# Kernel optimization log

Measured on AMD Instinct MI355X. Metric: run time of the kernel, lower is better.

Reference implementation:

```python
import jax, jax.numpy as jnp
import numpy as np

PHI = (1.0 + 5.0 ** 0.5) / 2.0
TWO_PI = 2.0 * np.pi
LN_EPS = 1e-5


def _complex_linear(xr, xi, Wr, Wi, br, bi):
    # (Wr + i*Wi) @ (xr + i*xi) + (br + i*bi)
    yr = xr @ Wr.T - xi @ Wi.T + br
    yi = xr @ Wi.T + xi @ Wr.T + bi
    return yr, yi


def _layernorm(x, g, b):
    m = jnp.mean(x, axis=-1, keepdims=True)
    v = jnp.mean((x - m) ** 2, axis=-1, keepdims=True)
    return (x - m) * jax.lax.rsqrt(v + LN_EPS) * g + b


def reference(w, b, ip_Wr, ip_Wi, ip_br, ip_bi, ln_g, ln_b, W_qkv, log_alpha, op_Wr, op_Wi):
    B, S, D = w.shape
    H = log_alpha.shape[0]
    Dh = D // H
    scale = jnp.sqrt(jnp.asarray(Dh, w.dtype))
    alpha = jax.nn.sigmoid(log_alpha)[None, :, None]  # (1,H,1)
    ts = jnp.arange(S, dtype=w.dtype)

    def step(carry, xs):
        hr, hi, vs = carry          # (B,D),(B,D),(B,H,Dh)
        w_t, b_t, t = xs            # (B,D),(B,D),()
        # InstrumentedEulerTransform: separated theta, complex product
        wl = 1.0 + jnp.abs(w_t)
        tphi = (t * PHI) % TWO_PI   # wrap_time_periodic
        thr = hr / wl + b_t + tphi
        thi = hi / wl + b_t + tphi
        sr, cr = jnp.sin(thr), jnp.cos(thr)
        si, ci = jnp.sin(thi), jnp.cos(thi)
        hr2 = cr * ci - sr * si
        hi2 = cr * si + sr * ci
        # InstrumentedEchoChamber.forward_step
        pr, pi_ = _complex_linear(hr2, hi2, ip_Wr, ip_Wi, ip_br, ip_bi)
        xc = _layernorm(pr + pi_, ln_g, ln_b)
        qkv = (xc @ W_qkv.T).reshape(B, 3, H, Dh)
        q, k, v = qkv[:, 0], qkv[:, 1], qkv[:, 2]
        vs2 = alpha * v + (1.0 - alpha) * vs
        gate = jax.nn.sigmoid(jnp.sum(q * k, axis=-1, keepdims=True) / scale)
        retr = (gate * vs2).reshape(B, D)
        # output_proj ComplexLinear on (retr, 0), no bias
        ore = retr @ op_Wr.T
        oim = retr @ op_Wi.T
        return (hr2, hi2, vs2), (ore, oim)

    init = (jnp.zeros((B, D), w.dtype), jnp.zeros((B, D), w.dtype),
            jnp.zeros((B, H, Dh), w.dtype))
    wT = jnp.swapaxes(w, 0, 1)  # (S,B,D)
    bT = jnp.swapaxes(b, 0, 1)
    _, (or_seq, oi_seq) = jax.lax.scan(step, init, (wT, bT, ts))
    out = jnp.stack([or_seq, oi_seq])      # (2,S,B,D)
    return jnp.swapaxes(out, 1, 2)         # (2,B,S,D)


def setup_inputs() -> dict:
    key = jax.random.key(0)
    ks = jax.random.split(key, 10)
    B, S, D, H = 8, 2048, 512, 8
    s = 0.02
    return {
        "w": jax.random.normal(ks[0], (B, S, D), jnp.float32),
        "b": jax.random.normal(ks[1], (B, S, D), jnp.float32),
        "ip_Wr": jax.random.normal(ks[2], (D, D), jnp.float32) * s,
        "ip_Wi": jax.random.normal(ks[3], (D, D), jnp.float32) * s,
        "ip_br": jax.random.normal(ks[4], (D,), jnp.float32) * s,
        "ip_bi": jax.random.normal(ks[5], (D,), jnp.float32) * s,
        "ln_g": jnp.ones((D,), jnp.float32),
        "ln_b": jnp.zeros((D,), jnp.float32),
        "W_qkv": jax.random.normal(ks[6], (3 * D, D), jnp.float32) * s,
        "log_alpha": jax.random.normal(ks[7], (H,), jnp.float32),
        "op_Wr": jax.random.normal(ks[8], (D, D), jnp.float32) * s,
        "op_Wi": jax.random.normal(ks[9], (D, D), jnp.float32) * s,
    }
```

## Files before the change

### kernel.cpp

```cpp
#include <hip/hip_runtime.h>
#include <math.h>

#define BB 8
#define SS 2048
#define DD 512
#define HH 8
#define MM (BB*SS)

#define CHK 64
#define CL  32
#define CW  64

#define RT 32
#define RW 128

typedef unsigned short u16;
typedef unsigned int   u32;
typedef float f32x4 __attribute__((ext_vector_type(4)));
typedef short s16x8 __attribute__((ext_vector_type(8)));

__device__ __forceinline__ u16 f2bf(float x){
  union { float f; unsigned u; } c; c.f = x;
  unsigned r = c.u + 0x7FFF + ((c.u >> 16) & 1);
  return (u16)(r >> 16);
}
__device__ __forceinline__ float bf2f(u16 x){
  union { unsigned u; float f; } c; c.u = ((unsigned)x) << 16;
  return c.f;
}
__device__ __forceinline__ void gload16(const u16* g, u16* l){
  __builtin_amdgcn_global_load_lds(
      (const __attribute__((address_space(1))) unsigned int*)g,
      (__attribute__((address_space(3))) unsigned int*)l, 16, 0, 0);
}

__global__ void prep_w1(const float* __restrict__ Wr, const float* __restrict__ Wi,
                        u16* __restrict__ W1){
  int id = blockIdx.x*256 + threadIdx.x;
  if (id >= 512*1024) return;
  int n = id >> 10, k = id & 1023;
  int d = k >> 1;
  float v = (k & 1) ? (Wr[n*512+d] - Wi[n*512+d])
                    : (Wr[n*512+d] + Wi[n*512+d]);
  W1[id] = f2bf(v);
}
__global__ void prep_wq(const float* __restrict__ Wq, u16* __restrict__ O){
  int id = blockIdx.x*256 + threadIdx.x;
  if (id >= 1536*512) return;
  O[id] = f2bf(Wq[id]);
}
__global__ void prep_w3(const float* __restrict__ Wor, const float* __restrict__ Woi,
                        u16* __restrict__ W3){
  int id = blockIdx.x*256 + threadIdx.x;
  if (id >= 1024*512) return;
  int n = id >> 9, k = id & 511;
  W3[id] = f2bf((n < 512) ? Wor[n*512+k] : Woi[(n-512)*512+k]);
}
__global__ void prep_misc(const float* __restrict__ br, const float* __restrict__ bi,
                          const float* __restrict__ la, float* __restrict__ bc,
                          float* __restrict__ alph){
  int t = threadIdx.x;
  if (t < 512) bc[t] = br[t] + bi[t];
  if (t < 8)   alph[t] = 1.0f/(1.0f + expf(-la[t]));
}
__global__ void prep_tphi(float* __restrict__ tphi2){
  int t = blockIdx.x*256 + threadIdx.x;
  if (t >= SS) return;
  const float PHI_F    = 1.61803398874989484820f;
  const float TWO_PI_F = 6.28318530717958647693f;
  tphi2[t] = 2.0f * fmodf((float)t * PHI_F, TWO_PI_F);
}

__global__ __launch_bounds__(256) void scan_h(const float* __restrict__ w,
                                              const float* __restrict__ bb,
                                              const float* __restrict__ tphi2,
                                              u32* __restrict__ X32){
  const int e = blockIdx.x*256 + threadIdx.x;
  const int c = blockIdx.y;
  const int b = e >> 9;
  const int d = e & 511;
  const float SQRT2 = 1.41421356237309504880f;
  const float PI_4  = 0.78539816339744830962f;
  const int tstart = c*CL;
  int t0 = tstart - CW; if (t0 < 0) t0 = 0;
  const int nw = tstart - t0;

  const float* wp = w  + ((size_t)b*SS + t0)*DD + d;
  const float* bp = bb + ((size_t)b*SS + t0)*DD + d;
  const float* tp = tphi2 + t0;

  float ss = 0.f;
  #pragma unroll 8
  for (int i=0;i<nw;i++){
    float wv = wp[(size_t)i*DD];
    float bv = bp[(size_t)i*DD];
    float rwl2 = SQRT2 * __builtin_amdgcn_rcpf(1.0f + fabsf(wv));
    float cw   = fmaf(2.0f, bv, tp[i]) + PI_4;
    ss = __sinf(fmaf(ss, rwl2, cw));
  }
  float hs = SQRT2 * ss;

  const float* wq = wp + (size_t)nw*DD;
  const float* bq = bp + (size_t)nw*DD;
  u32* xp = X32 + (size_t)(b*SS + tstart)*512 + d;
  #pragma unroll 8
  for (int i=0;i<CL;i++){
    float wv = wq[(size_t)i*DD];
    float bv = bq[(size_t)i*DD];
    float rwl = __builtin_amdgcn_rcpf(1.0f + fabsf(wv));
    float cc  = fmaf(2.0f, bv, tp[nw+i]);
    float theta = fmaf(hs, rwl, cc);
    float sn = __sinf(theta);
    float cs = __cosf(theta);
    hs = cs + sn;
    xp[(size_t)i*512] = (u32)f2bf(cs) | ((u32)f2bf(sn) << 16);
  }
}

template<int TAG, int EPI>
__global__ __launch_bounds__(256) void gemm_bf16(const u16* __restrict__ A,
                                                 const u16* __restrict__ W,
                                                 float* __restrict__ C0,
                                                 float* __restrict__ C1,
                                                 u16* __restrict__ C2,
                                                 int N, int K){
  __shared__ __align__(16) u16 As[2][128*32];
  __shared__ __align__(16) u16 Bs[2][128*32];
  const int tid  = threadIdx.x;
  const int nwgx = gridDim.x;
  const int nwg  = nwgx * gridDim.y;
  const int lin  = blockIdx.y * nwgx + blockIdx.x;
  const int qq   = nwg >> 3;
  const int logi = (lin & 7) * qq + (lin >> 3);
  const int m0   = (logi / nwgx) * 128;
  const int n0   = (logi % nwgx) * 128;

  const int wave = tid >> 6;
  const int lane = tid & 63;
  const int wr   = wave >> 1, wc = wave & 1;
  const int l15  = lane & 15;
  const int g    = lane >> 4;

  const int rI   = lane >> 2;
  const int kgs  = (lane & 3) ^ ((lane >> 3) & 3);
  const int row0 = (wave*2+0)*16 + rI;
  const int row1 = (wave*2+1)*16 + rI;
  const u16* Asrc0 = A + (size_t)(m0 + row0) * K + kgs*8;
  const u16* Asrc1 = A + (size_t)(m0 + row1) * K + kgs*8;
  const u16* Bsrc0 = W + (size_t)(n0 + row0) * K + kgs*8;
  const u16* Bsrc1 = W + (size_t)(n0 + row1) * K + kgs*8;
  const int ld0 = (wave*2+0)*512;
  const int ld1 = (wave*2+1)*512;

  f32x4 acc[4][4];
  #pragma unroll
  for (int i=0;i<4;i++)
    #pragma unroll
    for (int j=0;j<4;j++) acc[i][j] = (f32x4){0.f,0.f,0.f,0.f};

#define STAGE(buf, koff) do {                      \
    gload16(Asrc0 + (koff), &As[buf][ld0]);        \
    gload16(Asrc1 + (koff), &As[buf][ld1]);        \
    gload16(Bsrc0 + (koff), &Bs[buf][ld0]);        \
    gload16(Bsrc1 + (koff), &Bs[buf][ld1]);        \
  } while(0)

#define COMPUTE(buf) do {                                            \
    s16x8 af[4], bf[4];                                              \
    _Pragma("unroll")                                                \
    for (int s=0;s<4;s++){                                           \
      int rA = wr*64 + s*16 + l15;                                   \
      af[s] = *(const s16x8*)&As[buf][rA*32 + ((g ^ ((rA>>1)&3))*8)];\
      int rB = wc*64 + s*16 + l15;                                   \
      bf[s] = *(const s16x8*)&Bs[buf][rB*32 + ((g ^ ((rB>>1)&3))*8)];\
    }                                                                \
    _Pragma("unroll")                                                \
    for (int mi=0;mi<4;mi++)                                         \
      _Pragma("unroll")                                              \
      for (int ni=0;ni<4;ni++)                                       \
        acc[mi][ni] = __builtin_amdgcn_mfma_f32_16x16x32_bf16(af[mi], bf[ni], acc[mi][ni], 0, 0, 0); \
  } while(0)

  STAGE(0, 0);
  __syncthreads();
  int cur = 0;
  for (int k0 = 32; k0 < K; k0 += 32){
    STAGE(cur^1, k0);
    COMPUTE(cur);
    __syncthreads();
    cur ^= 1;
  }
  COMPUTE(cur);

#undef STAGE
#undef COMPUTE

  #pragma unroll
  for (int mi=0;mi<4;mi++){
    #pragma unroll
    for (int j=0;j<4;j++){
      int r = m0 + wr*64 + mi*16 + g*4 + j;
      #pragma unroll
      for (int ni=0;ni<4;ni++){
        int col = n0 + wc*64 + ni*16 + l15;
        float v = acc[mi][ni][j];
        if (EPI == 1){
          if (col < 512) C0[(size_t)r*512 + col]       = v;
          else           C1[(size_t)r*512 + (col-512)] = v;
        } else {
          C2[(size_t)r*N + col] = f2bf(v);
        }
      }
    }
  }
}

__global__ __launch_bounds__(256) void ln_kernel(const u16* __restrict__ y,
                                                 const float* __restrict__ bc,
                                                 const float* __restrict__ g,
                                                 const float* __restrict__ bb,
                                                 u16* __restrict__ xc){
  const int row  = blockIdx.x*4 + (threadIdx.x >> 6);
  const int lane = threadIdx.x & 63;
  s16x8 v = *(const s16x8*)(y + (size_t)row*512 + lane*8);
  float4 c0 = ((const float4*)bc)[lane*2];
  float4 c1 = ((const float4*)bc)[lane*2+1];
  float f[8];
  f[0] = bf2f((u16)v[0]) + c0.x; f[1] = bf2f((u16)v[1]) + c0.y;
  f[2] = bf2f((u16)v[2]) + c0.z; f[3] = bf2f((u16)v[3]) + c0.w;
  f[4] = bf2f((u16)v[4]) + c1.x; f[5] = bf2f((u16)v[5]) + c1.y;
  f[6] = bf2f((u16)v[6]) + c1.z; f[7] = bf2f((u16)v[7]) + c1.w;
  float s = 0.f, s2 = 0.f;
  #pragma unroll
  for (int i=0;i<8;i++){ s += f[i]; s2 = fmaf(f[i], f[i], s2); }
  #pragma unroll
  for (int off=32; off>0; off>>=1){ s += __shfl_xor(s, off); s2 += __shfl_xor(s2, off); }
  float mean = s * (1.0f/512.0f);
  float var  = s2 * (1.0f/512.0f) - mean*mean;
  float rstd = rsqrtf(var + 1e-5f);
  float4 g0 = ((const float4*)g)[lane*2],  g1 = ((const float4*)g)[lane*2+1];
  float4 b0 = ((const float4*)bb)[lane*2], b1 = ((const float4*)bb)[lane*2+1];
  s16x8 o;
  o[0] = (short)f2bf((f[0]-mean)*rstd*g0.x + b0.x);
  o[1] = (short)f2bf((f[1]-mean)*rstd*g0.y + b0.y);
  o[2] = (short)f2bf((f[2]-mean)*rstd*g0.z + b0.z);
  o[3] = (short)f2bf((f[3]-mean)*rstd*g0.w + b0.w);
  o[4] = (short)f2bf((f[4]-mean)*rstd*g1.x + b1.x);
  o[5] = (short)f2bf((f[5]-mean)*rstd*g1.y + b1.y);
  o[6] = (short)f2bf((f[6]-mean)*rstd*g1.z + b1.z);
  o[7] = (short)f2bf((f[7]-mean)*rstd*g1.w + b1.w);
  *(s16x8*)(xc + (size_t)row*512 + lane*8) = o;
}

__global__ __launch_bounds__(256) void retr_fused(const u16* __restrict__ qkv,
                                                  const float* __restrict__ alph,
                                                  u16* __restrict__ retr){
  const int wid  = blockIdx.x*4 + (threadIdx.x >> 6);
  const int lane = threadIdx.x & 63;
  const int c = wid & 63;
  const int h = (wid >> 6) & 7;
  const int b = wid >> 9;
  const float a  = alph[h];
  const float om = 1.0f - a;
  const int d  = h*64 + lane;
  const int t0 = c*RT;
  int w0 = t0 - RW; if (w0 < 0) w0 = 0;
  const int nw = t0 - w0;

  const u16* vp = qkv + ((size_t)(b*SS + w0))*1536 + 1024 + d;
  float vs = 0.f;
  #pragma unroll 8
  for (int i=0;i<nw;i++){
    vs = fmaf(a, bf2f(vp[(size_t)i*1536]), om*vs);
  }
  const u16* qp = qkv + ((size_t)(b*SS + t0))*1536 + d;
  u16* op = retr + ((size_t)(b*SS + t0))*512 + d;
  #pragma unroll 4
  for (int i=0;i<RT;i++){
    float q  = bf2f(qp[(size_t)i*1536]);
    float kk = bf2f(qp[(size_t)i*1536 + 512]);
    float v  = bf2f(qp[(size_t)i*1536 + 1024]);
    vs = fmaf(a, v, om*vs);
    float p = q*kk;
    #pragma unroll
    for (int off=32; off>0; off>>=1) p += __shfl_xor(p, off);
    float gate = 1.0f/(1.0f + __expf(-p*0.125f));
    op[(size_t)i*512] = f2bf(gate * vs);
  }
}

extern "C" void kernel_launch(void* const* d_in, const int* in_sizes, int n_in,
                              void* d_out, int out_size, void* d_ws, size_t ws_size,
                              hipStream_t stream) {
  const float* w    = (const float*)d_in[0];
  const float* b    = (const float*)d_in[1];
  const float* ipWr = (const float*)d_in[2];
  const float* ipWi = (const float*)d_in[3];
  const float* ipbr = (const float*)d_in[4];
  const float* ipbi = (const float*)d_in[5];
  const float* lng  = (const float*)d_in[6];
  const float* lnb  = (const float*)d_in[7];
  const float* Wqkv = (const float*)d_in[8];
  const float* la   = (const float*)d_in[9];
  const float* opWr = (const float*)d_in[10];
  const float* opWi = (const float*)d_in[11];
  float* out0 = (float*)d_out;
  float* out1 = out0 + (size_t)MM*DD;

  char* base = (char*)d_ws;
  u16*   W1    = (u16*)  (base + 0);
  u16*   Wq    = (u16*)  (base + 1048576);
  u16*   W3    = (u16*)  (base + 2621440);
  float* bc    = (float*)(base + 3670016);
  float* alph  = (float*)(base + 3672064);
  float* tphi2 = (float*)(base + 3672128);
  u32*   X32   = (u32*)  (base + 3680384);
  u16*   y     = (u16*)  (base + 37234816);
  u16*   xc    = (u16*)  (base + 54012032);
  u16*   qkv   = (u16*)  (base + 70789248);
  u16*   retr  = (u16*)X32;

  prep_w1 <<<2048,256,0,stream>>>(ipWr, ipWi, W1);
  prep_wq <<<3072,256,0,stream>>>(Wqkv, Wq);
  prep_w3 <<<2048,256,0,stream>>>(opWr, opWi, W3);
  prep_misc<<<1,512,0,stream>>>(ipbr, ipbi, la, bc, alph);
  prep_tphi<<<8,256,0,stream>>>(tphi2);

  scan_h<<<dim3(16,CHK),256,0,stream>>>(w, b, tphi2, X32);

  gemm_bf16<1,2><<<dim3(4,128),256,0,stream>>>((const u16*)X32, W1, nullptr, nullptr, y, 512, 1024);
  ln_kernel<<<4096,256,0,stream>>>(y, bc, lng, lnb, xc);
  gemm_bf16<2,2><<<dim3(12,128),256,0,stream>>>(xc, Wq, nullptr, nullptr, qkv, 1536, 512);

  retr_fused<<<1024,256,0,stream>>>(qkv, alph, retr);

  gemm_bf16<3,1><<<dim3(8,128),256,0,stream>>>(retr, W3, out0, out1, nullptr, 1024, 512);
}
```

Baseline: 181.1 us.

## Fuse prep kernels, shrink scan warmup window, software-prefetch scan loads

Merges the five weight and constant preparation kernels into one launch to cut launch overhead. Shrinks the warmup window of the chunked hidden-state scan from 64 to 48 steps, which reduces redundant recomputation but relies on the contraction forgetting the initial state within fewer steps. It also adds explicit register double-buffering of the strided w/b loads in scan_h and of the v loads in retr_fused, so memory latency overlaps the serial sin/fma chains.

```diff
diff --git a/kernel.cpp b/kernel.cpp
--- a/kernel.cpp
+++ b/kernel.cpp
@@ -9,7 +9,7 @@
 
 #define CHK 64
 #define CL  32
-#define CW  64
+#define CW  48
 
 #define RT 32
 #define RW 128
@@ -34,41 +34,40 @@
       (__attribute__((address_space(3))) unsigned int*)l, 16, 0, 0);
 }
 
-__global__ void prep_w1(const float* __restrict__ Wr, const float* __restrict__ Wi,
-                        u16* __restrict__ W1){
+__global__ void prep_all(const float* __restrict__ ipWr, const float* __restrict__ ipWi,
+                         const float* __restrict__ Wqkv,
+                         const float* __restrict__ opWr, const float* __restrict__ opWi,
+                         const float* __restrict__ ipbr, const float* __restrict__ ipbi,
+                         const float* __restrict__ la,
+                         u16* __restrict__ W1, u16* __restrict__ Wq, u16* __restrict__ W3,
+                         float* __restrict__ tphi2, float* __restrict__ bc,
+                         float* __restrict__ alph){
   int id = blockIdx.x*256 + threadIdx.x;
-  if (id >= 512*1024) return;
-  int n = id >> 10, k = id & 1023;
-  int d = k >> 1;
-  float v = (k & 1) ? (Wr[n*512+d] - Wi[n*512+d])
-                    : (Wr[n*512+d] + Wi[n*512+d]);
-  W1[id] = f2bf(v);
-}
-__global__ void prep_wq(const float* __restrict__ Wq, u16* __restrict__ O){
-  int id = blockIdx.x*256 + threadIdx.x;
-  if (id >= 1536*512) return;
-  O[id] = f2bf(Wq[id]);
-}
-__global__ void prep_w3(const float* __restrict__ Wor, const float* __restrict__ Woi,
-                        u16* __restrict__ W3){
-  int id = blockIdx.x*256 + threadIdx.x;
-  if (id >= 1024*512) return;
-  int n = id >> 9, k = id & 511;
-  W3[id] = f2bf((n < 512) ? Wor[n*512+k] : Woi[(n-512)*512+k]);
-}
-__global__ void prep_misc(const float* __restrict__ br, const float* __restrict__ bi,
-                          const float* __restrict__ la, float* __restrict__ bc,
-                          float* __restrict__ alph){
-  int t = threadIdx.x;
-  if (t < 512) bc[t] = br[t] + bi[t];
-  if (t < 8)   alph[t] = 1.0f/(1.0f + expf(-la[t]));
-}
-__global__ void prep_tphi(float* __restrict__ tphi2){
-  int t = blockIdx.x*256 + threadIdx.x;
-  if (t >= SS) return;
-  const float PHI_F    = 1.61803398874989484820f;
-  const float TWO_PI_F = 6.28318530717958647693f;
-  tphi2[t] = 2.0f * fmodf((float)t * PHI_F, TWO_PI_F);
+  if (id < 524288){
+    int n = id >> 10, k = id & 1023;
+    int d = k >> 1;
+    float v = (k & 1) ? (ipWr[n*512+d] - ipWi[n*512+d])
+                      : (ipWr[n*512+d] + ipWi[n*512+d]);
+    W1[id] = f2bf(v);
+  } else if (id < 1310720){
+    int i = id - 524288;
+    Wq[i] = f2bf(Wqkv[i]);
+  } else if (id < 1835008){
+    int i = id - 1310720;
+    int n = i >> 9, k = i & 511;
+    W3[i] = f2bf((n < 512) ? opWr[n*512+k] : opWi[(n-512)*512+k]);
+  } else if (id < 1837056){
+    int t = id - 1835008;
+    const float PHI_F    = 1.61803398874989484820f;
+    const float TWO_PI_F = 6.28318530717958647693f;
+    tphi2[t] = 2.0f * fmodf((float)t * PHI_F, TWO_PI_F);
+  } else if (id < 1837568){
+    int t = id - 1837056;
+    bc[t] = ipbr[t] + ipbi[t];
+  } else if (id < 1837576){
+    int t = id - 1837568;
+    alph[t] = 1.0f/(1.0f + expf(-la[t]));
+  }
 }
 
 __global__ __launch_bounds__(256) void scan_h(const float* __restrict__ w,
@@ -89,31 +88,59 @@
   const float* bp = bb + ((size_t)b*SS + t0)*DD + d;
   const float* tp = tphi2 + t0;
 
+  const int U = 8;
+  float wv[U], bv[U], wn[U], bn[U];
+
   float ss = 0.f;
-  #pragma unroll 8
-  for (int i=0;i<nw;i++){
-    float wv = wp[(size_t)i*DD];
-    float bv = bp[(size_t)i*DD];
-    float rwl2 = SQRT2 * __builtin_amdgcn_rcpf(1.0f + fabsf(wv));
-    float cw   = fmaf(2.0f, bv, tp[i]) + PI_4;
-    ss = __sinf(fmaf(ss, rwl2, cw));
+  const int ngw = nw >> 3;
+  if (ngw > 0){
+    #pragma unroll
+    for (int i=0;i<U;i++){ wv[i] = wp[(size_t)i*DD]; bv[i] = bp[(size_t)i*DD]; }
+    for (int gg=0; gg<ngw; ++gg){
+      if (gg+1 < ngw){
+        const float* wnp = wp + (size_t)(gg+1)*U*DD;
+        const float* bnp = bp + (size_t)(gg+1)*U*DD;
+        #pragma unroll
+        for (int i=0;i<U;i++){ wn[i] = wnp[(size_t)i*DD]; bn[i] = bnp[(size_t)i*DD]; }
+      }
+      #pragma unroll
+      for (int i=0;i<U;i++){
+        float rwl2 = SQRT2 * __builtin_amdgcn_rcpf(1.0f + fabsf(wv[i]));
+        float cw   = fmaf(2.0f, bv[i], tp[gg*U+i]) + PI_4;
+        ss = __sinf(fmaf(ss, rwl2, cw));
+      }
+      #pragma unroll
+      for (int i=0;i<U;i++){ wv[i]=wn[i]; bv[i]=bn[i]; }
+    }
   }
   float hs = SQRT2 * ss;
 
   const float* wq = wp + (size_t)nw*DD;
   const float* bq = bp + (size_t)nw*DD;
+  const float* tq = tp + nw;
   u32* xp = X32 + (size_t)(b*SS + tstart)*512 + d;
-  #pragma unroll 8
-  for (int i=0;i<CL;i++){
-    float wv = wq[(size_t)i*DD];
-    float bv = bq[(size_t)i*DD];
-    float rwl = __builtin_amdgcn_rcpf(1.0f + fabsf(wv));
-    float cc  = fmaf(2.0f, bv, tp[nw+i]);
-    float theta = fmaf(hs, rwl, cc);
-    float sn = __sinf(theta);
-    float cs = __cosf(theta);
-    hs = cs + sn;
-    xp[(size_t)i*512] = (u32)f2bf(cs) | ((u32)f2bf(sn) << 16);
+
+  #pragma unroll
+  for (int i=0;i<U;i++){ wv[i] = wq[(size_t)i*DD]; bv[i] = bq[(size_t)i*DD]; }
+  for (int gg=0; gg<CL/U; ++gg){
+    if (gg+1 < CL/U){
+      const float* wnp = wq + (size_t)(gg+1)*U*DD;
+      const float* bnp = bq + (size_t)(gg+1)*U*DD;
+      #pragma unroll
+      for (int i=0;i<U;i++){ wn[i] = wnp[(size_t)i*DD]; bn[i] = bnp[(size_t)i*DD]; }
+    }
+    #pragma unroll
+    for (int i=0;i<U;i++){
+      float rwl = __builtin_amdgcn_rcpf(1.0f + fabsf(wv[i]));
+      float cc  = fmaf(2.0f, bv[i], tq[gg*U+i]);
+      float theta = fmaf(hs, rwl, cc);
+      float sn = __sinf(theta);
+      float cs = __cosf(theta);
+      hs = cs + sn;
+      xp[(size_t)(gg*U+i)*512] = (u32)f2bf(cs) | ((u32)f2bf(sn) << 16);
+    }
+    #pragma unroll
+    for (int i=0;i<U;i++){ wv[i]=wn[i]; bv[i]=bn[i]; }
   }
 }
 
@@ -269,9 +296,25 @@
 
   const u16* vp = qkv + ((size_t)(b*SS + w0))*1536 + 1024 + d;
   float vs = 0.f;
-  #pragma unroll 8
-  for (int i=0;i<nw;i++){
-    vs = fmaf(a, bf2f(vp[(size_t)i*1536]), om*vs);
+  {
+    const int U = 8;
+    float vv[U], vn[U];
+    const int ng = nw >> 3;
+    if (ng > 0){
+      #pragma unroll
+      for (int i=0;i<U;i++) vv[i] = bf2f(vp[(size_t)i*1536]);
+      for (int gg=0; gg<ng; ++gg){
+        if (gg+1 < ng){
+          const u16* vnp = vp + (size_t)(gg+1)*U*1536;
+          #pragma unroll
+          for (int i=0;i<U;i++) vn[i] = bf2f(vnp[(size_t)i*1536]);
+        }
+        #pragma unroll
+        for (int i=0;i<U;i++) vs = fmaf(a, vv[i], om*vs);
+        #pragma unroll
+        for (int i=0;i<U;i++) vv[i] = vn[i];
+      }
+    }
   }
   const u16* qp = qkv + ((size_t)(b*SS + t0))*1536 + d;
   u16* op = retr + ((size_t)(b*SS + t0))*512 + d;
@@ -320,11 +363,8 @@
   u16*   qkv   = (u16*)  (base + 70789248);
   u16*   retr  = (u16*)X32;
 
-  prep_w1 <<<2048,256,0,stream>>>(ipWr, ipWi, W1);
-  prep_wq <<<3072,256,0,stream>>>(Wqkv, Wq);
-  prep_w3 <<<2048,256,0,stream>>>(opWr, opWi, W3);
-  prep_misc<<<1,512,0,stream>>>(ipbr, ipbi, la, bc, alph);
-  prep_tphi<<<8,256,0,stream>>>(tphi2);
+  prep_all<<<7179,256,0,stream>>>(ipWr, ipWi, Wqkv, opWr, opWi, ipbr, ipbi, la,
+                                  W1, Wq, W3, tphi2, bc, alph);
 
   scan_h<<<dim3(16,CHK),256,0,stream>>>(w, b, tphi2, X32);
 
```

Measured after the change: 166.0 us. 1.09x faster.
